# Kernel optimization log

Hardware: AMD Instinct MI355X
Metric: run time of the kernel (lower is better)

Reference implementation:

```python
import jax, jax.numpy as jnp
import numpy as np

N_CODE = 1024
D_K = 512
K = 16
BETA = (0.25, 1.0)
N_SMAT = 2
N = 32768


def setup_inputs() -> dict:
    key = jax.random.key(0)
    k1, k2, k3, k4, k5, k6 = jax.random.split(key, 6)
    x = jax.random.normal(k1, (1, N, D_K), dtype=jnp.float32)
    c = jax.random.normal(k2, (N_CODE, D_K), dtype=jnp.float32)
    # trans linears: Linear(n_code, n_code // 2**i) for i = 1..n_smat
    s = 1.0 / np.sqrt(N_CODE)
    W1 = jax.random.uniform(k3, (N_CODE // 2, N_CODE), jnp.float32, -s, s)
    b1 = jax.random.uniform(k4, (N_CODE // 2,), jnp.float32, -s, s)
    W2 = jax.random.uniform(k5, (N_CODE // 4, N_CODE), jnp.float32, -s, s)
    b2 = jax.random.uniform(k6, (N_CODE // 4,), jnp.float32, -s, s)
    return {"x": x, "c": c, "W1": W1, "b1": b1, "W2": W2, "b2": b2,
            "training": 1, "get_k": 0}


def _quantize(x, cb):
    # argmin of squared euclidean distance == argmin of cdist (p=2)
    # d2[n, m] = ||x_n||^2 - 2 x_n . c_m + ||c_m||^2
    d2 = (jnp.sum(x * x, axis=1, keepdims=True)
          - 2.0 * (x @ cb.T)
          + jnp.sum(cb * cb, axis=1))
    z = jnp.argmin(d2, axis=1)
    return z, cb[z]


def _vq_loss(z_q, x):
    # mse(z_q, sg(x)) and mse(x, sg(z_q)); values identical in forward
    e = jnp.mean((z_q - x) ** 2)
    return BETA[0] * e + BETA[1] * e


def reference(x, c, W1, b1, W2, b2, training, get_k):
    x2 = x[0]  # squeeze(0) -> [N, d_k]

    main_z, main_z_q = _quantize(x2, c)

    # sub-scale codebooks: L(c.T).T == W @ c + b[:, None]
    sub_z_q = jnp.zeros_like(main_z_q)
    for W, b in ((W1, b1), (W2, b2)):
        sub_c = W @ c + b[:, None]  # [n_code // 2^i, d_k]
        _, sub_q = _quantize(x2, sub_c)
        sub_z_q = sub_z_q + sub_q
    sub_z_q = sub_z_q / N_SMAT

    if training:
        total_loss = _vq_loss(main_z_q, x2) + _vq_loss(sub_z_q, x2)
    else:
        total_loss = jnp.zeros(())

    # get_k=0 path: ms_k_i stays zeros
    ms_k_i = jnp.zeros((K, D_K), dtype=x2.dtype)

    # unique rows of main_z_q == number of distinct codebook indices used
    counts = jnp.zeros((N_CODE,), jnp.int32).at[main_z].add(1)
    unique_rows = jnp.sum(counts > 0)

    # straight-through (values unchanged in forward)
    main_out = (x2 + jax.lax.stop_gradient(main_z_q - x2))[None]
    sub_out = (x2 + jax.lax.stop_gradient(sub_z_q - x2))[None]
    return main_out, sub_out, total_loss, ms_k_i, unique_rows
```

## Files before the change

kernel.cpp:

```cpp
#include <hip/hip_runtime.h>
#include <cstdint>

typedef unsigned short ushort_t;
typedef unsigned int uint_t;
typedef _Float16 f16x8 __attribute__((ext_vector_type(8)));
typedef float f32x4 __attribute__((ext_vector_type(4)));

#define N_ROWS 32768
#define DK 512
#define NC_MAIN 1024
#define NCB 1792
#define NTILE 14
#define NBLK_RG 8192

#define MAIN_OFF 0
#define SUB_OFF  16777216
#define LOSS_OFF 33554432
#define MSK_OFF  33554433
#define UNIQ_OFF 33562625

__device__ __forceinline__ uint_t umin_(uint_t a, uint_t b) { return a < b ? a : b; }
__device__ __forceinline__ uint_t umax_(uint_t a, uint_t b) { return a > b ? a : b; }

__global__ __launch_bounds__(256) void build_subcb(
    const float* __restrict__ c, const float* __restrict__ W1,
    const float* __restrict__ b1, const float* __restrict__ W2,
    const float* __restrict__ b2, float* __restrict__ CB,
    _Float16* __restrict__ cbh)
{
    int tid = threadIdx.x;
    int tx = tid & 63, ty = tid >> 6;
    int col = blockIdx.x * 64 + tx;
    int row0 = blockIdx.y * 16 + ty * 4;
    if (row0 < 1024) {
#pragma unroll
        for (int r = 0; r < 4; ++r) {
            float v = c[(row0 + r) * DK + col];
            CB[(row0 + r) * DK + col] = v;
            cbh[(row0 + r) * DK + col] = (_Float16)v;
        }
    } else {
        int i0 = row0 - 1024;
        const float* W;
        const float* b;
        if (i0 < 512) { W = W1; b = b1; }
        else          { W = W2; b = b2; i0 -= 512; }
        float acc[4] = {0.f, 0.f, 0.f, 0.f};
#pragma unroll 8
        for (int j = 0; j < 1024; ++j) {
            float cv = c[j * DK + col];
#pragma unroll
            for (int r = 0; r < 4; ++r)
                acc[r] += W[(i0 + r) * 1024 + j] * cv;
        }
#pragma unroll
        for (int r = 0; r < 4; ++r) {
            float v = acc[r] + b[i0 + r];
            CB[(row0 + r) * DK + col] = v;
            cbh[(row0 + r) * DK + col] = (_Float16)v;
        }
    }
}

__global__ __launch_bounds__(64) void row_norms(const float* __restrict__ CB,
                                                float* __restrict__ norms) {
    int row = blockIdx.x;
    int lane = threadIdx.x;
    const float4* p = (const float4*)(CB + (size_t)row * DK);
    float s = 0.f;
#pragma unroll
    for (int i = lane; i < 128; i += 64) {
        float4 v = p[i];
        s += v.x * v.x + v.y * v.y + v.z * v.z + v.w * v.w;
    }
#pragma unroll
    for (int off = 32; off; off >>= 1) s += __shfl_down(s, off, 64);
    if (lane == 0) norms[row] = s;
}

__global__ __launch_bounds__(256) void cvt_x(const float* __restrict__ in,
                                             _Float16* __restrict__ out,
                                             int* __restrict__ used) {
    int i = blockIdx.x * 256 + threadIdx.x;
    if (i < 1024) used[i] = 0;
    const float4* p = (const float4*)in + (size_t)i * 2;
    float4 a = p[0], b = p[1];
    f16x8 o;
    o[0] = (_Float16)a.x; o[1] = (_Float16)a.y; o[2] = (_Float16)a.z; o[3] = (_Float16)a.w;
    o[4] = (_Float16)b.x; o[5] = (_Float16)b.y; o[6] = (_Float16)b.z; o[7] = (_Float16)b.w;
    *((f16x8*)out + i) = o;
}

__device__ __forceinline__ void async16(void* lds, const void* g) {
    __builtin_amdgcn_global_load_lds(
        (const __attribute__((address_space(1))) unsigned int*)(uintptr_t)g,
        (__attribute__((address_space(3))) unsigned int*)(uintptr_t)lds,
        16, 0, 0);
}

__global__ __launch_bounds__(256) void gemm_topk(
    const _Float16* __restrict__ xh, const _Float16* __restrict__ cbh,
    const float* __restrict__ norms, uint2* __restrict__ candbuf)
{
    __shared__ __align__(16) ushort_t As[2][128 * 32];
    __shared__ __align__(16) ushort_t Bs[2][128 * 32];
    __shared__ uint2 cand[128][2];

    const int tid = threadIdx.x;
    const int lane = tid & 63;
    const int wid = tid >> 6;
    const int wy = wid >> 1, wx = wid & 1;
    const int lane15 = lane & 15, q = lane >> 4;

    const int bid = blockIdx.y * NTILE + blockIdx.x;
    const int xcd = bid & 7;
    const int slot = bid >> 3;
    const int tileN = slot % NTILE;
    const int rowG = slot / NTILE;
    const int rowBase = (rowG * 8 + xcd) * 128;
    const int c0 = tileN * 128;

    size_t aoff[2], boff[2];
    int ldsoff[2];
#pragma unroll
    for (int i = 0; i < 2; ++i) {
        int gid = i * 256 + tid;
        int row = gid >> 2;
        int gp = gid & 3;
        int gsw = gp ^ (row & 3);
        aoff[i] = (size_t)(rowBase + row) * DK + gsw * 8;
        boff[i] = (size_t)(c0 + row) * DK + gsw * 8;
        ldsoff[i] = gid * 8;
    }

    int rA[4], rB[4];
#pragma unroll
    for (int t = 0; t < 4; ++t) {
        rA[t] = wy * 64 + t * 16 + lane15;
        rB[t] = wx * 64 + t * 16 + lane15;
    }

    f32x4 acc[4][4];
#pragma unroll
    for (int mr = 0; mr < 4; ++mr)
#pragma unroll
        for (int nc = 0; nc < 4; ++nc) acc[mr][nc] = (f32x4)0.f;

#pragma unroll
    for (int i = 0; i < 2; ++i) {
        async16(&As[0][ldsoff[i]], xh + aoff[i]);
        async16(&Bs[0][ldsoff[i]], cbh + boff[i]);
    }

#pragma unroll
    for (int it = 0; it < 16; ++it) {
        const int cur = it & 1;
        __syncthreads();
        if (it < 15) {
            const int nxt = cur ^ 1;
            const int kk = (it + 1) * 32;
#pragma unroll
            for (int i = 0; i < 2; ++i) {
                async16(&As[nxt][ldsoff[i]], xh + aoff[i] + kk);
                async16(&Bs[nxt][ldsoff[i]], cbh + boff[i] + kk);
            }
        }
        f16x8 av[4], bv[4];
#pragma unroll
        for (int mr = 0; mr < 4; ++mr)
            av[mr] = *(const f16x8*)&As[cur][rA[mr] * 32 + (q ^ (rA[mr] & 3)) * 8];
#pragma unroll
        for (int nc = 0; nc < 4; ++nc)
            bv[nc] = *(const f16x8*)&Bs[cur][rB[nc] * 32 + (q ^ (rB[nc] & 3)) * 8];
#pragma unroll
        for (int mr = 0; mr < 4; ++mr)
#pragma unroll
            for (int nc = 0; nc < 4; ++nc)
                acc[mr][nc] = __builtin_amdgcn_mfma_f32_16x16x32_f16(
                    av[mr], bv[nc], acc[mr][nc], 0, 0, 0);
    }

    float nrm[4];
    uint_t colGlob[4];
#pragma unroll
    for (int nc = 0; nc < 4; ++nc) {
        colGlob[nc] = (uint_t)(c0 + wx * 64 + nc * 16 + lane15);
        nrm[nc] = norms[colGlob[nc]];
    }

#pragma unroll
    for (int mr = 0; mr < 4; ++mr) {
#pragma unroll
        for (int r = 0; r < 4; ++r) {
            uint_t k[4];
#pragma unroll
            for (int nc = 0; nc < 4; ++nc) {
                float s = fmaf(-2.f, acc[mr][nc][r], nrm[nc]);
                uint_t b = __float_as_uint(s);
                uint_t u = b ^ ((uint_t)((int)b >> 31) | 0x80000000u);
                k[nc] = (u & 0xFFFFF800u) | colGlob[nc];
            }
            uint_t lo01 = umin_(k[0], k[1]), hi01 = umax_(k[0], k[1]);
            uint_t lo23 = umin_(k[2], k[3]), hi23 = umax_(k[2], k[3]);
            uint_t k1 = umin_(lo01, lo23);
            uint_t k2 = umin_(umin_(hi01, hi23), umax_(lo01, lo23));
#pragma unroll
            for (int m = 1; m <= 8; m <<= 1) {
                uint_t o1 = __shfl_xor(k1, m, 64);
                uint_t o2 = __shfl_xor(k2, m, 64);
                uint_t n1 = umin_(k1, o1);
                uint_t n2 = umin_(umax_(k1, o1), umin_(k2, o2));
                k1 = n1; k2 = n2;
            }
            if (lane15 == 0) {
                int rloc = wy * 64 + mr * 16 + q * 4 + r;
                cand[rloc][wx] = make_uint2(k1, k2);
            }
        }
    }
    __syncthreads();
    if (tid < 128) {
        uint2 a = cand[tid][0], b = cand[tid][1];
        uint_t k1 = umin_(a.x, b.x);
        uint_t k2 = umin_(umax_(a.x, b.x), umin_(a.y, b.y));
        candbuf[(size_t)(rowBase + tid) * NTILE + tileN] = make_uint2(k1, k2);
    }
}

__device__ __forceinline__ void push4u(uint_t v, uint_t* bs) {
#pragma unroll
    for (int j = 0; j < 4; ++j) {
        uint_t lo = umin_(v, bs[j]);
        uint_t hi = umax_(v, bs[j]);
        bs[j] = lo; v = hi;
    }
}

__global__ __launch_bounds__(256) void rescue_gather(
    const float* __restrict__ x, const float* __restrict__ CB,
    const float* __restrict__ norms, const uint2* __restrict__ candbuf,
    float* __restrict__ main_out, float* __restrict__ sub_out,
    float2* __restrict__ lossPart, int* __restrict__ used)
{
    const int lane = threadIdx.x & 63;
    const int wv = threadIdx.x >> 6;
    const int r = blockIdx.x * 4 + wv;

    const float4* xp = (const float4*)(x + (size_t)r * DK) + lane * 2;
    float4 xa = xp[0], xb = xp[1];

    const uint2* cbp = candbuf + (size_t)r * NTILE;

    int si[12];
    {
        uint_t bs[4];
#pragma unroll
        for (int j = 0; j < 4; ++j) bs[j] = 0xFFFFFFFFu;
#pragma unroll
        for (int t = 0; t < 8; ++t) {
            uint2 e = cbp[t];
            push4u(__builtin_amdgcn_readfirstlane(e.x), bs);
            push4u(__builtin_amdgcn_readfirstlane(e.y), bs);
        }
#pragma unroll
        for (int j = 0; j < 4; ++j) si[j] = (int)(bs[j] & 2047u);
#pragma unroll
        for (int j = 0; j < 4; ++j) bs[j] = 0xFFFFFFFFu;
#pragma unroll
        for (int t = 8; t < 12; ++t) {
            uint2 e = cbp[t];
            push4u(__builtin_amdgcn_readfirstlane(e.x), bs);
            push4u(__builtin_amdgcn_readfirstlane(e.y), bs);
        }
#pragma unroll
        for (int j = 0; j < 4; ++j) si[4 + j] = (int)(bs[j] & 2047u);
#pragma unroll
        for (int j = 0; j < 4; ++j) bs[j] = 0xFFFFFFFFu;
#pragma unroll
        for (int t = 12; t < 14; ++t) {
            uint2 e = cbp[t];
            push4u(__builtin_amdgcn_readfirstlane(e.x), bs);
            push4u(__builtin_amdgcn_readfirstlane(e.y), bs);
        }
#pragma unroll
        for (int j = 0; j < 4; ++j) si[8 + j] = (int)(bs[j] & 2047u);
    }

    float d[12];
#pragma unroll
    for (int k = 0; k < 12; ++k) {
        const float4* cp = (const float4*)(CB + (size_t)si[k] * DK) + lane * 2;
        float4 a = cp[0], b = cp[1];
        d[k] = xa.x * a.x + xa.y * a.y + xa.z * a.z + xa.w * a.w
             + xb.x * b.x + xb.y * b.y + xb.z * b.z + xb.w * b.w;
    }
#pragma unroll
    for (int off = 32; off; off >>= 1)
#pragma unroll
        for (int k = 0; k < 12; ++k) d[k] += __shfl_xor(d[k], off, 64);

    float sc[12];
#pragma unroll
    for (int k = 0; k < 12; ++k) sc[k] = norms[si[k]] - 2.f * d[k];

    int pick[3];
#pragma unroll
    for (int g = 0; g < 3; ++g) {
        float bv = sc[g * 4]; int bidx = si[g * 4];
#pragma unroll
        for (int k = 1; k < 4; ++k) {
            float v = sc[g * 4 + k]; int idx = si[g * 4 + k];
            if (v < bv || (v == bv && idx < bidx)) { bv = v; bidx = idx; }
        }
        pick[g] = bidx;
    }
    const int A = pick[0], B = pick[1], C = pick[2];

    const float4* pa = (const float4*)(CB + (size_t)A * DK) + lane * 2;
    const float4* pb = (const float4*)(CB + (size_t)B * DK) + lane * 2;
    const float4* pc = (const float4*)(CB + (size_t)C * DK) + lane * 2;
    float4* mo = (float4*)(main_out + (size_t)r * DK) + lane * 2;
    float4* so = (float4*)(sub_out + (size_t)r * DK) + lane * 2;
    float em = 0.f, es = 0.f;
#pragma unroll
    for (int i = 0; i < 2; ++i) {
        float4 xq = (i == 0) ? xa : xb;
        float4 cm = pa[i];
        float4 q1 = pb[i];
        float4 q2 = pc[i];
        float4 cs;
        cs.x = 0.5f * (q1.x + q2.x);
        cs.y = 0.5f * (q1.y + q2.y);
        cs.z = 0.5f * (q1.z + q2.z);
        cs.w = 0.5f * (q1.w + q2.w);
        mo[i] = cm;
        so[i] = cs;
        float t;
        t = cm.x - xq.x; em += t * t;
        t = cm.y - xq.y; em += t * t;
        t = cm.z - xq.z; em += t * t;
        t = cm.w - xq.w; em += t * t;
        t = cs.x - xq.x; es += t * t;
        t = cs.y - xq.y; es += t * t;
        t = cs.z - xq.z; es += t * t;
        t = cs.w - xq.w; es += t * t;
    }
#pragma unroll
    for (int off = 32; off; off >>= 1) {
        em += __shfl_down(em, off, 64);
        es += __shfl_down(es, off, 64);
    }
    __shared__ float sm[8];
    if (lane == 0) {
        sm[wv] = em; sm[4 + wv] = es;
        used[A] = 1;
    }
    __syncthreads();
    if (threadIdx.x == 0) {
        lossPart[blockIdx.x] = make_float2(sm[0] + sm[1] + sm[2] + sm[3],
                                           sm[4] + sm[5] + sm[6] + sm[7]);
    }
}

__global__ __launch_bounds__(256) void finalize_kernel(
    const int* __restrict__ used, const float2* __restrict__ lossPart,
    const int* __restrict__ training, float* __restrict__ out)
{
    int tid = threadIdx.x;
    int cnt = 0;
    for (int i = tid; i < 1024; i += 256) cnt += (used[i] != 0);
    float em = 0.f, es = 0.f;
    for (int i = tid; i < NBLK_RG; i += 256) {
        float2 p = lossPart[i];
        em += p.x; es += p.y;
    }
#pragma unroll
    for (int off = 32; off; off >>= 1) {
        cnt += __shfl_down(cnt, off, 64);
        em += __shfl_down(em, off, 64);
        es += __shfl_down(es, off, 64);
    }
    __shared__ int sc[4];
    __shared__ float se[4], ss[4];
    if ((tid & 63) == 0) { sc[tid >> 6] = cnt; se[tid >> 6] = em; ss[tid >> 6] = es; }
    __syncthreads();
    if (tid == 0) {
        int total = sc[0] + sc[1] + sc[2] + sc[3];
        float tl = 0.f;
        if (*training) {
            float l0 = se[0] + se[1] + se[2] + se[3];
            float l1 = ss[0] + ss[1] + ss[2] + ss[3];
            tl = 1.25f * (l0 + l1) * (1.0f / ((float)N_ROWS * (float)DK));
        }
        out[LOSS_OFF] = tl;
        out[UNIQ_OFF] = (float)total;
    }
    for (int i = tid; i < 8192; i += 256) out[MSK_OFF + i] = 0.f;
}

extern "C" void kernel_launch(void* const* d_in, const int* in_sizes, int n_in,
                              void* d_out, int out_size, void* d_ws, size_t ws_size,
                              hipStream_t stream) {
    const float* x = (const float*)d_in[0];
    const float* c = (const float*)d_in[1];
    const float* W1 = (const float*)d_in[2];
    const float* b1 = (const float*)d_in[3];
    const float* W2 = (const float*)d_in[4];
    const float* b2 = (const float*)d_in[5];
    const int* training = (const int*)d_in[6];
    float* out = (float*)d_out;

    char* p = (char*)d_ws;
    float* CB = (float*)p;          p += (size_t)NCB * DK * 4;
    _Float16* xh = (_Float16*)p;    p += (size_t)N_ROWS * DK * 2;
    _Float16* cbh = (_Float16*)p;   p += (size_t)NCB * DK * 2;
    uint2* candbuf = (uint2*)p;     p += (size_t)N_ROWS * NTILE * 8;
    float* norms = (float*)p;       p += NCB * 4;
    float2* lossPart = (float2*)p;  p += (size_t)NBLK_RG * 8;
    int* used = (int*)p;            p += 4096;

    build_subcb<<<dim3(8, 112), dim3(256), 0, stream>>>(c, W1, b1, W2, b2, CB, cbh);
    row_norms<<<dim3(NCB), dim3(64), 0, stream>>>(CB, norms);
    cvt_x<<<dim3(8192), dim3(256), 0, stream>>>(x, xh, used);
    gemm_topk<<<dim3(NTILE, 256), dim3(256), 0, stream>>>(xh, cbh, norms, candbuf);
    rescue_gather<<<dim3(NBLK_RG), dim3(256), 0, stream>>>(
        x, CB, norms, candbuf, out + MAIN_OFF, out + SUB_OFF, lossPart, used);
    finalize_kernel<<<dim3(1), dim3(256), 0, stream>>>(used, lossPart, training, out);
}
```

Measured before the change: 415.7 us.

## Merge codebook build and x conversion into one prep kernel, use nontemporal gather I/O

Merges build_subcb and cvt_x into a single prep_kernel launch and moves the ms_k zero-fill there from finalize. rescue_gather now processes 8 rows per 512-thread block, which halves the number of loss partials. x, candbuf and the output stores use nontemporal loads and stores to avoid polluting the cache. The intent is to remove one launch and overlap the sub-codebook GEMM with the x conversion, with little change to the dominant GEMM kernel.

```diff
diff --git a/kernel.cpp b/kernel.cpp
--- a/kernel.cpp
+++ b/kernel.cpp
@@ -5,13 +5,14 @@
 typedef unsigned int uint_t;
 typedef _Float16 f16x8 __attribute__((ext_vector_type(8)));
 typedef float f32x4 __attribute__((ext_vector_type(4)));
+typedef uint_t u32x2 __attribute__((ext_vector_type(2)));
 
 #define N_ROWS 32768
 #define DK 512
 #define NC_MAIN 1024
 #define NCB 1792
 #define NTILE 14
-#define NBLK_RG 8192
+#define NBLK_RG 4096
 
 #define MAIN_OFF 0
 #define SUB_OFF  16777216
@@ -22,43 +23,71 @@
 __device__ __forceinline__ uint_t umin_(uint_t a, uint_t b) { return a < b ? a : b; }
 __device__ __forceinline__ uint_t umax_(uint_t a, uint_t b) { return a > b ? a : b; }
 
-__global__ __launch_bounds__(256) void build_subcb(
+__device__ __forceinline__ float4 ntld4(const float4* p) {
+    f32x4 v = __builtin_nontemporal_load((const f32x4*)p);
+    return make_float4(v[0], v[1], v[2], v[3]);
+}
+__device__ __forceinline__ void ntst4(float4* p, float4 v) {
+    f32x4 t; t[0] = v.x; t[1] = v.y; t[2] = v.z; t[3] = v.w;
+    __builtin_nontemporal_store(t, (f32x4*)p);
+}
+__device__ __forceinline__ uint2 ntld2(const uint2* p) {
+    u32x2 v = __builtin_nontemporal_load((const u32x2*)p);
+    return make_uint2(v[0], v[1]);
+}
+
+__global__ __launch_bounds__(256) void prep_kernel(
     const float* __restrict__ c, const float* __restrict__ W1,
     const float* __restrict__ b1, const float* __restrict__ W2,
     const float* __restrict__ b2, float* __restrict__ CB,
-    _Float16* __restrict__ cbh)
+    _Float16* __restrict__ cbh,
+    const float* __restrict__ x, _Float16* __restrict__ xh,
+    int* __restrict__ used, float* __restrict__ out)
 {
-    int tid = threadIdx.x;
-    int tx = tid & 63, ty = tid >> 6;
-    int col = blockIdx.x * 64 + tx;
-    int row0 = blockIdx.y * 16 + ty * 4;
-    if (row0 < 1024) {
-#pragma unroll
-        for (int r = 0; r < 4; ++r) {
-            float v = c[(row0 + r) * DK + col];
-            CB[(row0 + r) * DK + col] = v;
-            cbh[(row0 + r) * DK + col] = (_Float16)v;
+    const int bid = blockIdx.x;
+    const int tid = threadIdx.x;
+    if (bid < 896) {
+        int tx = tid & 63, ty = tid >> 6;
+        int col = (bid & 7) * 64 + tx;
+        int row0 = (bid >> 3) * 16 + ty * 4;
+        if (row0 < 1024) {
+#pragma unroll
+            for (int r = 0; r < 4; ++r) {
+                float v = c[(row0 + r) * DK + col];
+                CB[(row0 + r) * DK + col] = v;
+                cbh[(row0 + r) * DK + col] = (_Float16)v;
+            }
+        } else {
+            int i0 = row0 - 1024;
+            const float* W;
+            const float* b;
+            if (i0 < 512) { W = W1; b = b1; }
+            else          { W = W2; b = b2; i0 -= 512; }
+            float acc[4] = {0.f, 0.f, 0.f, 0.f};
+#pragma unroll 8
+            for (int j = 0; j < 1024; ++j) {
+                float cv = c[j * DK + col];
+#pragma unroll
+                for (int r = 0; r < 4; ++r)
+                    acc[r] += W[(i0 + r) * 1024 + j] * cv;
+            }
+#pragma unroll
+            for (int r = 0; r < 4; ++r) {
+                float v = acc[r] + b[i0 + r];
+                CB[(row0 + r) * DK + col] = v;
+                cbh[(row0 + r) * DK + col] = (_Float16)v;
+            }
         }
     } else {
-        int i0 = row0 - 1024;
-        const float* W;
-        const float* b;
-        if (i0 < 512) { W = W1; b = b1; }
-        else          { W = W2; b = b2; i0 -= 512; }
-        float acc[4] = {0.f, 0.f, 0.f, 0.f};
-#pragma unroll 8
-        for (int j = 0; j < 1024; ++j) {
-            float cv = c[j * DK + col];
-#pragma unroll
-            for (int r = 0; r < 4; ++r)
-                acc[r] += W[(i0 + r) * 1024 + j] * cv;
-        }
-#pragma unroll
-        for (int r = 0; r < 4; ++r) {
-            float v = acc[r] + b[i0 + r];
-            CB[(row0 + r) * DK + col] = v;
-            cbh[(row0 + r) * DK + col] = (_Float16)v;
-        }
+        int i = (bid - 896) * 256 + tid;
+        if (i < 1024) used[i] = 0;
+        if (i < 8192) out[MSK_OFF + i] = 0.f;
+        const float4* p = (const float4*)x + (size_t)i * 2;
+        float4 a = p[0], b = p[1];
+        f16x8 o;
+        o[0] = (_Float16)a.x; o[1] = (_Float16)a.y; o[2] = (_Float16)a.z; o[3] = (_Float16)a.w;
+        o[4] = (_Float16)b.x; o[5] = (_Float16)b.y; o[6] = (_Float16)b.z; o[7] = (_Float16)b.w;
+        *((f16x8*)xh + i) = o;
     }
 }
 
@@ -76,19 +105,6 @@
 #pragma unroll
     for (int off = 32; off; off >>= 1) s += __shfl_down(s, off, 64);
     if (lane == 0) norms[row] = s;
-}
-
-__global__ __launch_bounds__(256) void cvt_x(const float* __restrict__ in,
-                                             _Float16* __restrict__ out,
-                                             int* __restrict__ used) {
-    int i = blockIdx.x * 256 + threadIdx.x;
-    if (i < 1024) used[i] = 0;
-    const float4* p = (const float4*)in + (size_t)i * 2;
-    float4 a = p[0], b = p[1];
-    f16x8 o;
-    o[0] = (_Float16)a.x; o[1] = (_Float16)a.y; o[2] = (_Float16)a.z; o[3] = (_Float16)a.w;
-    o[4] = (_Float16)b.x; o[5] = (_Float16)b.y; o[6] = (_Float16)b.z; o[7] = (_Float16)b.w;
-    *((f16x8*)out + i) = o;
 }
 
 __device__ __forceinline__ void async16(void* lds, const void* g) {
@@ -236,7 +252,7 @@
     }
 }
 
-__global__ __launch_bounds__(256) void rescue_gather(
+__global__ __launch_bounds__(512) void rescue_gather(
     const float* __restrict__ x, const float* __restrict__ CB,
     const float* __restrict__ norms, const uint2* __restrict__ candbuf,
     float* __restrict__ main_out, float* __restrict__ sub_out,
@@ -244,10 +260,10 @@
 {
     const int lane = threadIdx.x & 63;
     const int wv = threadIdx.x >> 6;
-    const int r = blockIdx.x * 4 + wv;
+    const int r = blockIdx.x * 8 + wv;
 
     const float4* xp = (const float4*)(x + (size_t)r * DK) + lane * 2;
-    float4 xa = xp[0], xb = xp[1];
+    float4 xa = ntld4(xp), xb = ntld4(xp + 1);
 
     const uint2* cbp = candbuf + (size_t)r * NTILE;
 
@@ -258,7 +274,7 @@
         for (int j = 0; j < 4; ++j) bs[j] = 0xFFFFFFFFu;
 #pragma unroll
         for (int t = 0; t < 8; ++t) {
-            uint2 e = cbp[t];
+            uint2 e = ntld2(&cbp[t]);
             push4u(__builtin_amdgcn_readfirstlane(e.x), bs);
             push4u(__builtin_amdgcn_readfirstlane(e.y), bs);
         }
@@ -268,7 +284,7 @@
         for (int j = 0; j < 4; ++j) bs[j] = 0xFFFFFFFFu;
 #pragma unroll
         for (int t = 8; t < 12; ++t) {
-            uint2 e = cbp[t];
+            uint2 e = ntld2(&cbp[t]);
             push4u(__builtin_amdgcn_readfirstlane(e.x), bs);
             push4u(__builtin_amdgcn_readfirstlane(e.y), bs);
         }
@@ -278,7 +294,7 @@
         for (int j = 0; j < 4; ++j) bs[j] = 0xFFFFFFFFu;
 #pragma unroll
         for (int t = 12; t < 14; ++t) {
-            uint2 e = cbp[t];
+            uint2 e = ntld2(&cbp[t]);
             push4u(__builtin_amdgcn_readfirstlane(e.x), bs);
             push4u(__builtin_amdgcn_readfirstlane(e.y), bs);
         }
@@ -333,8 +349,8 @@
         cs.y = 0.5f * (q1.y + q2.y);
         cs.z = 0.5f * (q1.z + q2.z);
         cs.w = 0.5f * (q1.w + q2.w);
-        mo[i] = cm;
-        so[i] = cs;
+        ntst4(&mo[i], cm);
+        ntst4(&so[i], cs);
         float t;
         t = cm.x - xq.x; em += t * t;
         t = cm.y - xq.y; em += t * t;
@@ -350,15 +366,17 @@
         em += __shfl_down(em, off, 64);
         es += __shfl_down(es, off, 64);
     }
-    __shared__ float sm[8];
+    __shared__ float sm[16];
     if (lane == 0) {
-        sm[wv] = em; sm[4 + wv] = es;
+        sm[wv] = em; sm[8 + wv] = es;
         used[A] = 1;
     }
     __syncthreads();
     if (threadIdx.x == 0) {
-        lossPart[blockIdx.x] = make_float2(sm[0] + sm[1] + sm[2] + sm[3],
-                                           sm[4] + sm[5] + sm[6] + sm[7]);
+        float e0 = 0.f, e1 = 0.f;
+#pragma unroll
+        for (int i = 0; i < 8; ++i) { e0 += sm[i]; e1 += sm[8 + i]; }
+        lossPart[blockIdx.x] = make_float2(e0, e1);
     }
 }
 
@@ -395,7 +413,6 @@
         out[LOSS_OFF] = tl;
         out[UNIQ_OFF] = (float)total;
     }
-    for (int i = tid; i < 8192; i += 256) out[MSK_OFF + i] = 0.f;
 }
 
 extern "C" void kernel_launch(void* const* d_in, const int* in_sizes, int n_in,
@@ -419,11 +436,11 @@
     float2* lossPart = (float2*)p;  p += (size_t)NBLK_RG * 8;
     int* used = (int*)p;            p += 4096;
 
-    build_subcb<<<dim3(8, 112), dim3(256), 0, stream>>>(c, W1, b1, W2, b2, CB, cbh);
+    prep_kernel<<<dim3(9088), dim3(256), 0, stream>>>(
+        c, W1, b1, W2, b2, CB, cbh, x, xh, used, out);
     row_norms<<<dim3(NCB), dim3(64), 0, stream>>>(CB, norms);
-    cvt_x<<<dim3(8192), dim3(256), 0, stream>>>(x, xh, used);
     gemm_topk<<<dim3(NTILE, 256), dim3(256), 0, stream>>>(xh, cbh, norms, candbuf);
-    rescue_gather<<<dim3(NBLK_RG), dim3(256), 0, stream>>>(
+    rescue_gather<<<dim3(NBLK_RG), dim3(512), 0, stream>>>(
         x, CB, norms, candbuf, out + MAIN_OFF, out + SUB_OFF, lossPart, used);
     finalize_kernel<<<dim3(1), dim3(256), 0, stream>>>(used, lossPart, training, out);
 }
```

After: 408.9 us. Within noise of the previous version (-1.6%).
